# Optimization experiments

Measured on AMD Instinct MI355X. Metric: run time of the kernel, lower is better.

Reference implementation:

```python
import jax, jax.numpy as jnp
import numpy as np
import math, itertools

# Problem sizes: N nodes, D feature dim, M max hyperedge cardinality,
# E hyperedges, B target nodes to aggregate for.
N, D, M, E, B = 50000, 128, 3, 200000, 16384


def _alpha(c, M):
    # sum of multinomial coefficients over positive integers (inclusion-exclusion)
    return sum((-1) ** i * math.comb(c, i) * (c - i) ** M for i in range(c))


def _build_hypergraph():
    """Generate a random hypergraph and precompute, for every target node, the
    flat list of M-1 length combinations and their scalar weights
    weight = adj_coef(c, node) * num_distinct_permutations(comb).
    This reproduces exactly the per-node/per-edge/per-combination math of
    TMessagePassing.aggregate_with_M / aggregate_with_c, hoisted to setup time.
    """
    rng = np.random.default_rng(0)
    card = rng.integers(2, M + 1, size=E)              # edge cardinality in {2, 3}
    r = rng.integers(0, N, size=E)
    o1 = rng.integers(1, 100, size=E)
    o2 = rng.integers(1, 100, size=E)
    full = np.stack([r, (r + o1) % N, (r + o1 + o2) % N], axis=1)  # distinct nodes

    structure = [[] for _ in range(N)]
    edge_nodes = []
    for i in range(E):
        e = full[i, : card[i]].tolist()
        edge_nodes.append(e)
        for v in e:
            structure[v].append(i)

    targets = np.arange(B, dtype=np.int64)
    all_combs, all_weights = [], []
    fact_M1 = math.factorial(M - 1)
    for t in targets:
        t = int(t)
        eids = structure[t]
        deg = len(eids)
        ci, cw = [], []
        for eid in eids:
            edge = edge_nodes[eid]
            c = len(edge)
            a = (c / _alpha(c, M)) / deg               # adj_coef(c, node)
            if c == M:
                tmp = edge.copy()
                tmp.remove(t)
                ci.append(tmp)
                cw.append(a * fact_M1)                 # num_perms = (M-1)!
            else:
                for comb in itertools.combinations_with_replacement(edge, M):
                    if set(comb) == set(edge):
                        tmp = list(comb)
                        tmp.remove(t)
                        counts = {}
                        for v in tmp:
                            counts[v] = counts.get(v, 0) + 1
                        nperm = fact_M1
                        for k in counts.values():
                            nperm //= math.factorial(k)
                        ci.append(tmp)
                        cw.append(a * nperm)
        all_combs.append(ci)
        all_weights.append(cw)

    cmax = max(1, max(len(c) for c in all_combs))
    comb_idx = np.zeros((B, cmax, M - 1), dtype=np.int32)
    comb_w = np.zeros((B, cmax), dtype=np.float32)     # 0 weight => padding
    has_edge = np.zeros((B,), dtype=np.float32)
    for b in range(B):
        for j, (ci, w) in enumerate(zip(all_combs[b], all_weights[b])):
            comb_idx[b, j] = ci
            comb_w[b, j] = w
        has_edge[b] = 1.0 if all_combs[b] else 0.0
    return targets, comb_idx, comb_w, has_edge


def setup_inputs() -> dict:
    key = jax.random.key(0)
    targets, comb_idx, comb_w, has_edge = _build_hypergraph()
    features = jax.random.normal(key, (N, D), dtype=jnp.float32)
    return {
        "features": features,
        "target_nodes": jnp.asarray(targets),
        "comb_idx": jnp.asarray(comb_idx),
        "comb_w": jnp.asarray(comb_w),
        "has_edge": jnp.asarray(has_edge),
    }


def reference(features, target_nodes, comb_idx, comb_w, has_edge):
    # gather: [B, C, M-1, D]
    g = features[comb_idx]
    # product of the M-1 gathered feature vectors: [B, C, D]
    prod = jnp.prod(g, axis=2)
    # weighted sum over combinations (adj_coef * num_perms baked into comb_w)
    agg = jnp.einsum("bc,bcd->bd", comb_w, prod)
    # nodes with no incident edges return their own feature (the `if not edges` branch)
    self_feat = features[target_nodes]
    return jnp.where(has_edge[:, None] > 0, agg, self_feat)
```

## Files before the change

kernel.cpp:

```cpp
#include <hip/hip_runtime.h>


typedef float vfloat4 __attribute__((ext_vector_type(4)));

template <bool REG_WIDX>
__global__ __launch_bounds__(256) void tmp_aggregate_kernel(
    const float*  __restrict__ features,
    const int*    __restrict__ target_nodes,
    const int*    __restrict__ comb_idx,
    const float*  __restrict__ comb_w,
    const float*  __restrict__ has_edge,
    float*        __restrict__ out,
    int B, int cmax)
{
    const int nwg = gridDim.x;
    const int xcd = blockIdx.x & 7;
    const int jj  = blockIdx.x >> 3;
    const int q   = nwg >> 3, r = nwg & 7;
    const int lb  = (xcd < r ? xcd * (q + 1) : r * (q + 1) + (xcd - r) * q) + jj;

    const int lane    = threadIdx.x & 63;
    const int wave    = __builtin_amdgcn_readfirstlane((int)(threadIdx.x >> 6));
    const int sub     = lane & 31;
    const int half    = lane >> 5;
    const int rowbase = (lb * 4 + wave) * 2;
    const int b       = rowbase + half;
    if (rowbase >= B) return;

    const vfloat4* __restrict__ f4   = (const vfloat4*)features;
    const int2*    __restrict__ idx2 = (const int2*)comb_idx;
    const long base = (long)b * cmax;

    const int tnode = target_nodes[b];
    const vfloat4 ft = f4[(tnode << 5) + sub];

    vfloat4 acc = {0.f, 0.f, 0.f, 0.f};

    if (REG_WIDX) {
        const bool v0 = (sub < cmax), v1 = (sub + 32 < cmax);
        const float w0 = v0 ? comb_w[base + sub]      : 0.f;
        const float w1 = v1 ? comb_w[base + sub + 32] : 0.f;
        const int2  i0 = v0 ? idx2[base + sub]        : make_int2(0, 0);
        const int2  i1 = v1 ? idx2[base + sub + 32]   : make_int2(0, 0);

        const unsigned long long m0 = __ballot(w0 != 0.f);
        const unsigned long long m1 = __ballot(w1 != 0.f);
        const int cnt = __popc((unsigned)(m0 >> (half * 32)))
                      + __popc((unsigned)(m1 >> (half * 32)));
        const int cnt_other = __shfl(cnt, lane ^ 32);
        const int loop_n = __builtin_amdgcn_readfirstlane(cnt > cnt_other ? cnt : cnt_other);

        #pragma unroll 4
        for (int c = 0; c < loop_n; ++c) {
            const int src = half * 32 + (c & 31);
            const float w   = __shfl(c < 32 ? w0   : w1,   src);
            const int   ixx = __shfl(c < 32 ? i0.x : i1.x, src);
            const int   ixy = __shfl(c < 32 ? i0.y : i1.y, src);
            const vfloat4 x = f4[(ixx << 5) + sub];
            const vfloat4 y = f4[(ixy << 5) + sub];
            acc.x = fmaf(w * x.x, y.x, acc.x);
            acc.y = fmaf(w * x.y, y.y, acc.y);
            acc.z = fmaf(w * x.z, y.z, acc.z);
            acc.w = fmaf(w * x.w, y.w, acc.w);
        }
    } else {
        int cnt = 0;
        for (int c0 = 0; c0 < cmax; c0 += 32) {
            const int c = c0 + sub;
            const float w = (c < cmax) ? comb_w[base + c] : 0.0f;
            const unsigned long long m = __ballot(w != 0.0f);
            cnt += __popc((unsigned)(m >> (half * 32)));
            const bool tail0 = ((unsigned)(m      ) != 0xffffffffu);
            const bool tail1 = ((unsigned)(m >> 32) != 0xffffffffu);
            if (tail0 && tail1) break;
        }
        const int cnt_other = __shfl(cnt, lane ^ 32);
        const int loop_n = __builtin_amdgcn_readfirstlane(cnt > cnt_other ? cnt : cnt_other);

        #pragma unroll 4
        for (int c = 0; c < loop_n; ++c) {
            const float w  = comb_w[base + c];
            const int2  ix = idx2[base + c];
            const vfloat4 x = f4[(ix.x << 5) + sub];
            const vfloat4 y = f4[(ix.y << 5) + sub];
            acc.x = fmaf(w * x.x, y.x, acc.x);
            acc.y = fmaf(w * x.y, y.y, acc.y);
            acc.z = fmaf(w * x.z, y.z, acc.z);
            acc.w = fmaf(w * x.w, y.w, acc.w);
        }
    }

    const bool fb = !(has_edge[b] > 0.f);
    acc.x = fb ? ft.x : acc.x;
    acc.y = fb ? ft.y : acc.y;
    acc.z = fb ? ft.z : acc.z;
    acc.w = fb ? ft.w : acc.w;

    __builtin_nontemporal_store(acc, &((vfloat4*)out)[(b << 5) + sub]);
}

extern "C" void kernel_launch(void* const* d_in, const int* in_sizes, int n_in,
                              void* d_out, int out_size, void* d_ws, size_t ws_size,
                              hipStream_t stream) {
    const float* features     = (const float*)d_in[0];
    const int*   target_nodes = (const int*)d_in[1];
    const int*   comb_idx     = (const int*)d_in[2];
    const float* comb_w       = (const float*)d_in[3];
    const float* has_edge     = (const float*)d_in[4];
    float*       out          = (float*)d_out;

    const int B    = in_sizes[1];
    const int cmax = in_sizes[2] / (B * 2);

    const int rows_per_block = 8;
    const int grid = (B + rows_per_block - 1) / rows_per_block;

    if (cmax <= 64) {
        tmp_aggregate_kernel<true><<<grid, 256, 0, stream>>>(
            features, target_nodes, comb_idx, comb_w, has_edge, out, B, cmax);
    } else {
        tmp_aggregate_kernel<false><<<grid, 256, 0, stream>>>(
            features, target_nodes, comb_idx, comb_w, has_edge, out, B, cmax);
    }
}
```

Measured before the change: 18.05 us.

## Merge paired cardinality-2 combinations via preprocess pass to reduce feature gathers

```diff
diff --git a/kernel.cpp b/kernel.cpp
--- a/kernel.cpp
+++ b/kernel.cpp
@@ -2,6 +2,129 @@
 
 
 typedef float vfloat4 __attribute__((ext_vector_type(4)));
+
+__global__ __launch_bounds__(64) void preprocess_kernel(
+    const int2*  __restrict__ idx2,
+    const float* __restrict__ w,
+    const int*   __restrict__ tn,
+    int*         __restrict__ rcnt,
+    int4*        __restrict__ rec,
+    int B, int cmax)
+{
+    const int b = blockIdx.x * 64 + threadIdx.x;
+    if (b >= B) return;
+    const long base = (long)b * cmax;
+    const int  t    = tn[b];
+
+    int c = 0, n = 0;
+    while (c < cmax) {
+        const float wc = w[base + c];
+        if (wc == 0.f) break;
+        const int2 ix = idx2[base + c];
+        bool merged = false;
+        if (c + 1 < cmax) {
+            const float wn = w[base + c + 1];
+            if (wn != 0.f) {
+                const int2 jx = idx2[base + c + 1];
+                if (ix.x == ix.y) {
+                    const int a = ix.x;
+                    if ((jx.x == t && jx.y == a) || (jx.y == t && jx.x == a)) {
+                        rec[base + n] = make_int4(a, a, __float_as_int(wn), __float_as_int(wc));
+                        ++n; c += 2; merged = true;
+                    }
+                } else if (jx.x == jx.y) {
+                    const int a = jx.x;
+                    if ((ix.x == t && ix.y == a) || (ix.y == t && ix.x == a)) {
+                        rec[base + n] = make_int4(a, a, __float_as_int(wc), __float_as_int(wn));
+                        ++n; c += 2; merged = true;
+                    }
+                }
+            }
+        }
+        if (!merged) {
+            int4 r;
+            if (ix.x == t)          r = make_int4(ix.y, ix.y, __float_as_int(wc), 0);
+            else if (ix.y == t)     r = make_int4(ix.x, ix.x, __float_as_int(wc), 0);
+            else if (ix.x == ix.y)  r = make_int4(ix.x, ix.x, 0, __float_as_int(wc));
+            else                    r = make_int4(ix.x, ix.y, 0, __float_as_int(wc));
+            rec[base + n] = r; ++n; c += 1;
+        }
+    }
+    rcnt[b] = n;
+}
+
+__global__ __launch_bounds__(256) void merged_aggregate_kernel(
+    const float* __restrict__ features,
+    const int*   __restrict__ target_nodes,
+    const int*   __restrict__ rcnt,
+    const int4*  __restrict__ rec,
+    const float* __restrict__ has_edge,
+    float*       __restrict__ out,
+    int B, int cmax)
+{
+    const int nwg = gridDim.x;
+    const int xcd = blockIdx.x & 7;
+    const int jj  = blockIdx.x >> 3;
+    const int q   = nwg >> 3, r = nwg & 7;
+    const int lb  = (xcd < r ? xcd * (q + 1) : r * (q + 1) + (xcd - r) * q) + jj;
+
+    const int lane    = threadIdx.x & 63;
+    const int wave    = __builtin_amdgcn_readfirstlane((int)(threadIdx.x >> 6));
+    const int sub     = lane & 31;
+    const int half    = lane >> 5;
+    const int rowbase = (lb * 4 + wave) * 2;
+    const int b       = rowbase + half;
+    if (rowbase >= B) return;
+
+    const vfloat4* __restrict__ f4 = (const vfloat4*)features;
+    const long rbase = (long)b * cmax;
+
+    const int tnode = target_nodes[b];
+    const vfloat4 ft = f4[(tnode << 5) + sub];
+
+    const int myrc = rcnt[b];
+    const int rc_other = __shfl(myrc, lane ^ 32);
+    const int loop_n = __builtin_amdgcn_readfirstlane(myrc > rc_other ? myrc : rc_other);
+
+    const int4 zero4 = make_int4(0, 0, 0, 0);
+    const int4 ra = (sub      < cmax) ? rec[rbase + sub]      : zero4;
+    const int4 rb = (sub + 32 < cmax) ? rec[rbase + sub + 32] : zero4;
+
+    vfloat4 acc = {0.f, 0.f, 0.f, 0.f};
+
+    #pragma unroll 4
+    for (int c = 0; c < loop_n; ++c) {
+        const int  src  = half * 32 + (c & 31);
+        const int4 rsel = (c < 32) ? ra : rb;
+        int   i0 = __shfl(rsel.x, src);
+        int   i1 = __shfl(rsel.y, src);
+        float wa = __shfl(__int_as_float(rsel.z), src);
+        float wb = __shfl(__int_as_float(rsel.w), src);
+
+        const bool valid = (c < myrc);
+        i0 = valid ? i0 : 0;
+        i1 = valid ? i1 : 0;
+        wa = valid ? wa : 0.f;
+        wb = valid ? wb : 0.f;
+
+        const vfloat4 x = f4[(i0 << 5) + sub];
+        const vfloat4 y = f4[(i1 << 5) + sub];
+
+        float t0;
+        t0 = fmaf(wb, y.x, wa * ft.x); acc.x = fmaf(x.x, t0, acc.x);
+        t0 = fmaf(wb, y.y, wa * ft.y); acc.y = fmaf(x.y, t0, acc.y);
+        t0 = fmaf(wb, y.z, wa * ft.z); acc.z = fmaf(x.z, t0, acc.z);
+        t0 = fmaf(wb, y.w, wa * ft.w); acc.w = fmaf(x.w, t0, acc.w);
+    }
+
+    const bool fb = !(has_edge[b] > 0.f);
+    acc.x = fb ? ft.x : acc.x;
+    acc.y = fb ? ft.y : acc.y;
+    acc.z = fb ? ft.z : acc.z;
+    acc.w = fb ? ft.w : acc.w;
+
+    __builtin_nontemporal_store(acc, &((vfloat4*)out)[(b << 5) + sub]);
+}
 
 template <bool REG_WIDX>
 __global__ __launch_bounds__(256) void tmp_aggregate_kernel(
@@ -115,7 +238,16 @@
     const int rows_per_block = 8;
     const int grid = (B + rows_per_block - 1) / rows_per_block;
 
-    if (cmax <= 64) {
+    const size_t need = (size_t)B * 4 + (size_t)B * cmax * 16;
+
+    if (cmax <= 64 && ws_size >= need) {
+        int*  rcnt = (int*)d_ws;
+        int4* rec  = (int4*)((char*)d_ws + (size_t)B * 4);
+        preprocess_kernel<<<(B + 63) / 64, 64, 0, stream>>>(
+            (const int2*)comb_idx, comb_w, target_nodes, rcnt, rec, B, cmax);
+        merged_aggregate_kernel<<<grid, 256, 0, stream>>>(
+            features, target_nodes, rcnt, rec, has_edge, out, B, cmax);
+    } else if (cmax <= 64) {
         tmp_aggregate_kernel<true><<<grid, 256, 0, stream>>>(
             features, target_nodes, comb_idx, comb_w, has_edge, out, B, cmax);
     } else {
```

Result: slower. 34.95 us (+93.7%).
